# Kernel tuning notes

Hardware: AMD Instinct MI355X
Metric: run time of the kernel (lower is better)

The kernel has to match this reference:

```python
import jax, jax.numpy as jnp
import numpy as np


def _gcn_layer(x, W, b, src, dst, norm, n_nodes):
    # x: [N, Fin]; transform first (PyG GCNConv): h = x @ W
    h = x @ W  # [N, Fout]
    # gather-scale-scatter: out[d] += norm_e * h[s] over edges (incl. self loops)
    msgs = h[src] * norm[:, None]  # [E+N, Fout]
    agg = jax.ops.segment_sum(msgs, dst, num_segments=n_nodes)
    return agg + b


def setup_inputs() -> dict:
    key = jax.random.key(0)
    k1, k2, k3, k4 = jax.random.split(key, 4)
    N, E, F_IN, HID, OUT = 50000, 800000, 128, 256, 128
    x = jax.random.normal(k1, (N, F_IN), dtype=jnp.float32)
    edge_index = jax.random.randint(k2, (2, E), 0, N, dtype=jnp.int64)
    W1 = jax.random.normal(k3, (F_IN, HID), dtype=jnp.float32) / np.sqrt(F_IN)
    b1 = jnp.zeros((HID,), dtype=jnp.float32)
    W2 = jax.random.normal(k4, (HID, OUT), dtype=jnp.float32) / np.sqrt(HID)
    b2 = jnp.zeros((OUT,), dtype=jnp.float32)
    return {"x": x, "edge_index": edge_index, "W1": W1, "b1": b1, "W2": W2, "b2": b2}


def reference(x, edge_index, W1, b1, W2, b2):
    N = x.shape[0]
    # GCN normalization with self loops: A_hat = D^-1/2 (A + I) D^-1/2
    self_loops = jnp.arange(N, dtype=edge_index.dtype)
    src = jnp.concatenate([edge_index[0], self_loops])
    dst = jnp.concatenate([edge_index[1], self_loops])
    deg = jax.ops.segment_sum(jnp.ones_like(dst, dtype=x.dtype), dst, num_segments=N)
    dinv = jnp.where(deg > 0, jax.lax.rsqrt(deg), 0.0)
    norm = dinv[src] * dinv[dst]  # [E+N]
    h = _gcn_layer(x, W1, b1, src, dst, norm, N)
    h = jax.nn.relu(h)  # dropout is identity in eval mode
    out = _gcn_layer(h, W2, b2, src, dst, norm, N)
    return out  # unsupervised mode returns raw embeddings [N, 128]
```

## Files before the change

### kernel.cpp

```cpp
#include <hip/hip_runtime.h>
#include <hip/hip_bf16.h>


static constexpr int N_NODES = 50000;
static constexpr int N_EDGES = 800000;
static constexpr int F_IN = 128;
static constexpr int HID  = 256;
static constexpr int F_OUT = 128;
static constexpr int H2P  = 258;

typedef __attribute__((ext_vector_type(8))) short short8;
typedef __attribute__((ext_vector_type(4))) float f32x4;

__device__ __forceinline__ unsigned short f2bf(float f) {
    union { float f; unsigned u; } x; x.f = f;
    unsigned r = x.u + 0x7FFF + ((x.u >> 16) & 1);
    return (unsigned short)(r >> 16);
}
__device__ __forceinline__ float bf2f(unsigned short h) {
    union { unsigned u; float f; } x; x.u = ((unsigned)h) << 16;
    return x.f;
}

__global__ void deg_wt_kernel(const int* __restrict__ dst, int* __restrict__ deg,
                              int* __restrict__ pos, int E,
                              const float* __restrict__ W1, unsigned short* __restrict__ w1t,
                              const float* __restrict__ W2, unsigned short* __restrict__ w2t,
                              int EB, int NB1) {
    const int b = blockIdx.x;
    if (b < EB) {
        int i = b * 256 + threadIdx.x;
        if (i < E) pos[i] = atomicAdd(&deg[dst[i]], 1);
    } else if (b < EB + NB1) {
        int t = (b - EB) * 256 + threadIdx.x;
        if (t < F_IN * HID) {
            int n = t / F_IN, k = t - n * F_IN;
            w1t[t] = f2bf(W1[(size_t)k * HID + n]);
        }
    } else {
        int t = (b - EB - NB1) * 256 + threadIdx.x;
        if (t < HID * F_OUT) {
            int n = t / HID, k = t - n * HID;
            w2t[t] = f2bf(W2[(size_t)k * F_OUT + n]);
        }
    }
}

__global__ __launch_bounds__(256) void scan_reduce_dinv(const int* __restrict__ deg,
                                                        int* __restrict__ bsums,
                                                        float* __restrict__ dinv, int N) {
    int i = blockIdx.x * 256 + threadIdx.x;
    int v = (i < N) ? deg[i] : 0;
    if (i < N) dinv[i] = rsqrtf((float)(v + 1));
#pragma unroll
    for (int ofs = 32; ofs > 0; ofs >>= 1) v += __shfl_down(v, ofs);
    __shared__ int ws[4];
    if ((threadIdx.x & 63) == 0) ws[threadIdx.x >> 6] = v;
    __syncthreads();
    if (threadIdx.x == 0) bsums[blockIdx.x] = ws[0] + ws[1] + ws[2] + ws[3];
}

__global__ __launch_bounds__(256) void scan_final_scalex(const int* __restrict__ deg,
                                                         const int* __restrict__ bsums,
                                                         int* __restrict__ off, int N, int nb,
                                                         const float* __restrict__ x,
                                                         const float* __restrict__ dinv,
                                                         unsigned short* __restrict__ xs) {
    const int tid = threadIdx.x;
    if ((int)blockIdx.x >= nb) {
        int i = (blockIdx.x - nb) * 256 + tid;
        if (i < N_NODES * F_IN / 8) {
            float dv = dinv[i >> 4];
            float4 v0 = ((const float4*)x)[i * 2];
            float4 v1 = ((const float4*)x)[i * 2 + 1];
            short8 o;
            o[0] = (short)f2bf(v0.x * dv); o[1] = (short)f2bf(v0.y * dv);
            o[2] = (short)f2bf(v0.z * dv); o[3] = (short)f2bf(v0.w * dv);
            o[4] = (short)f2bf(v1.x * dv); o[5] = (short)f2bf(v1.y * dv);
            o[6] = (short)f2bf(v1.z * dv); o[7] = (short)f2bf(v1.w * dv);
            *(short8*)(xs + (size_t)i * 8) = o;
        }
        return;
    }
    __shared__ int bs[256];
    __shared__ int s[256];
    bs[tid] = (tid < nb) ? bsums[tid] : 0;
    const int i = blockIdx.x * 256 + tid;
    int v = (i < N) ? deg[i] : 0;
    s[tid] = v;
    __syncthreads();
    for (int ofs = 1; ofs < 256; ofs <<= 1) {
        int tb = (tid >= ofs) ? bs[tid - ofs] : 0;
        int tv = (tid >= ofs) ? s[tid - ofs] : 0;
        __syncthreads();
        bs[tid] += tb;
        s[tid] += tv;
        __syncthreads();
    }
    int bbase = (blockIdx.x == 0) ? 0 : bs[blockIdx.x - 1];
    int excl = (tid == 0) ? 0 : s[tid - 1];
    if (i <= N) off[i] = bbase + excl;
}

__global__ void scatter_kernel(const int* __restrict__ src, const int* __restrict__ dst,
                               const int* __restrict__ pos, const int* __restrict__ off,
                               int* __restrict__ csr, int E) {
    int i = blockIdx.x * blockDim.x + threadIdx.x;
    if (i < E) csr[off[dst[i]] + pos[i]] = src[i];
}

template <int MODE>
__global__ __launch_bounds__(256) void agg_bf16(const unsigned short* __restrict__ hs,
                                                const int* __restrict__ off,
                                                const int* __restrict__ csr,
                                                const float* __restrict__ dinv,
                                                const float* __restrict__ bias,
                                                void* __restrict__ outp, int N) {
    const int wid = threadIdx.x >> 6;
    const int n = blockIdx.x * 4 + wid;
    if (n >= N) return;
    const int lane = threadIdx.x & 63;
    const int lane16 = lane & 15;
    const int slot = lane >> 4;

    float va[8], vb[8], vc[8], vd[8];
#pragma unroll
    for (int j = 0; j < 8; j++) { va[j] = 0.f; vb[j] = 0.f; vc[j] = 0.f; vd[j] = 0.f; }

    if (slot == 0) {
        short8 s = *(const short8*)(hs + (size_t)n * 128 + lane16 * 8);
#pragma unroll
        for (int j = 0; j < 8; j++) va[j] = bf2f((unsigned short)s[j]);
    }

    const int e0 = off[n];
    const int e1 = off[n + 1];
    for (int e = e0 + slot; e < e1; e += 16) {
        const int i1 = e + 4, i2 = e + 8, i3 = e + 12;
        const float f1 = (i1 < e1) ? 1.f : 0.f;
        const float f2 = (i2 < e1) ? 1.f : 0.f;
        const float f3 = (i3 < e1) ? 1.f : 0.f;
        const int c1 = min(i1, e1 - 1), c2 = min(i2, e1 - 1), c3 = min(i3, e1 - 1);
        int s0 = csr[e];
        int s1 = csr[c1];
        int s2 = csr[c2];
        int s3 = csr[c3];
        short8 v0 = *(const short8*)(hs + (size_t)s0 * 128 + lane16 * 8);
        short8 v1 = *(const short8*)(hs + (size_t)s1 * 128 + lane16 * 8);
        short8 v2 = *(const short8*)(hs + (size_t)s2 * 128 + lane16 * 8);
        short8 v3 = *(const short8*)(hs + (size_t)s3 * 128 + lane16 * 8);
#pragma unroll
        for (int j = 0; j < 8; j++) va[j] += bf2f((unsigned short)v0[j]);
#pragma unroll
        for (int j = 0; j < 8; j++) vb[j] = fmaf(f1, bf2f((unsigned short)v1[j]), vb[j]);
#pragma unroll
        for (int j = 0; j < 8; j++) vc[j] = fmaf(f2, bf2f((unsigned short)v2[j]), vc[j]);
#pragma unroll
        for (int j = 0; j < 8; j++) vd[j] = fmaf(f3, bf2f((unsigned short)v3[j]), vd[j]);
    }
#pragma unroll
    for (int j = 0; j < 8; j++) va[j] += vb[j] + vc[j] + vd[j];

#pragma unroll
    for (int j = 0; j < 8; j++) va[j] += __shfl_down(va[j], 32);
#pragma unroll
    for (int j = 0; j < 8; j++) va[j] += __shfl_down(va[j], 16);

    if (lane < 16) {
        float dv = dinv[n];
        if (MODE == 0) {
            short8 o;
#pragma unroll
            for (int j = 0; j < 8; j++) o[j] = (short)f2bf(va[j] * dv);
            *(short8*)((unsigned short*)outp + (size_t)n * 128 + lane * 8) = o;
        } else {
            float* op = (float*)outp + (size_t)n * 128 + lane * 8;
            float4 o0, o1;
            o0.x = va[0] * dv + bias[lane * 8 + 0];
            o0.y = va[1] * dv + bias[lane * 8 + 1];
            o0.z = va[2] * dv + bias[lane * 8 + 2];
            o0.w = va[3] * dv + bias[lane * 8 + 3];
            o1.x = va[4] * dv + bias[lane * 8 + 4];
            o1.y = va[5] * dv + bias[lane * 8 + 5];
            o1.z = va[6] * dv + bias[lane * 8 + 6];
            o1.w = va[7] * dv + bias[lane * 8 + 7];
            ((float4*)op)[0] = o0;
            ((float4*)op)[1] = o1;
        }
    }
}

__global__ __launch_bounds__(512, 4) void gemm12(const unsigned short* __restrict__ Y,
                                                 const unsigned short* __restrict__ w1t,
                                                 const float* __restrict__ b1,
                                                 const unsigned short* __restrict__ w2t,
                                                 const float* __restrict__ dinv,
                                                 unsigned short* __restrict__ hs2, int M) {
    __shared__ unsigned short h2s[16 * H2P];

    const int wid = threadIdx.x >> 6;
    const int lane = threadIdx.x & 63;
    const int an = lane & 15;
    const int q = lane >> 4;

    short8 b1f[2][4];
    float bv[2];
#pragma unroll
    for (int t = 0; t < 2; t++) {
        const int col = wid * 32 + t * 16 + an;
        const unsigned short* wp = w1t + (size_t)col * F_IN + q * 8;
#pragma unroll
        for (int c = 0; c < 4; c++) b1f[t][c] = *(const short8*)(wp + c * 32);
        bv[t] = b1[col];
    }
    short8 b2f[8];
    const int colB = wid * 16 + an;
    {
        const unsigned short* wp = w2t + (size_t)colB * HID + q * 8;
#pragma unroll
        for (int c = 0; c < 8; c++) b2f[c] = *(const short8*)(wp + c * 32);
    }

    const int T = M >> 4;
    for (int t0 = blockIdx.x; t0 < T; t0 += gridDim.x) {
        const int m0 = t0 * 16;

        short8 a[4];
        {
            const unsigned short* yp = Y + (size_t)(m0 + an) * F_IN + q * 8;
#pragma unroll
            for (int c = 0; c < 4; c++) a[c] = *(const short8*)(yp + c * 32);
        }
        f32x4 accA0 = {0.f, 0.f, 0.f, 0.f};
        f32x4 accA1 = {0.f, 0.f, 0.f, 0.f};
#pragma unroll
        for (int c = 0; c < 4; c++) {
            accA0 = __builtin_amdgcn_mfma_f32_16x16x32_bf16(a[c], b1f[0][c], accA0, 0, 0, 0);
            accA1 = __builtin_amdgcn_mfma_f32_16x16x32_bf16(a[c], b1f[1][c], accA1, 0, 0, 0);
        }
        {
            const int c0 = wid * 32 + an;
            unsigned short* hrow = &h2s[(q * 4) * H2P];
#pragma unroll
            for (int rr = 0; rr < 4; rr++) {
                hrow[rr * H2P + c0]      = f2bf(fmaxf(accA0[rr] + bv[0], 0.f));
                hrow[rr * H2P + c0 + 16] = f2bf(fmaxf(accA1[rr] + bv[1], 0.f));
            }
        }
        __syncthreads();

        {
            short8 h[8];
            const unsigned short* hp = &h2s[an * H2P + q * 8];
#pragma unroll
            for (int c = 0; c < 8; c++) h[c] = *(const short8*)(hp + c * 32);
            f32x4 acc = {0.f, 0.f, 0.f, 0.f};
#pragma unroll
            for (int c = 0; c < 8; c++)
                acc = __builtin_amdgcn_mfma_f32_16x16x32_bf16(h[c], b2f[c], acc, 0, 0, 0);
            const float4 dv4 = ((const float4*)dinv)[(m0 >> 2) + q];
            unsigned short* op = hs2 + (size_t)(m0 + q * 4) * F_OUT + colB;
            op[0]         = f2bf(acc[0] * dv4.x);
            op[F_OUT]     = f2bf(acc[1] * dv4.y);
            op[2 * F_OUT] = f2bf(acc[2] * dv4.z);
            op[3 * F_OUT] = f2bf(acc[3] * dv4.w);
        }
        __syncthreads();
    }
}

extern "C" void kernel_launch(void* const* d_in, const int* in_sizes, int n_in,
                              void* d_out, int out_size, void* d_ws, size_t ws_size,
                              hipStream_t stream) {
    const float* x  = (const float*)d_in[0];
    const int*   ei = (const int*)d_in[1];
    const float* W1 = (const float*)d_in[2];
    const float* b1 = (const float*)d_in[3];
    const float* W2 = (const float*)d_in[4];
    const float* b2 = (const float*)d_in[5];

    const int N = N_NODES;
    const int E = N_EDGES;
    const int* srcp = ei;
    const int* dstp = ei + E;

    char* base = (char*)d_ws;
    size_t o = 0;
    auto alloc = [&](size_t bytes) {
        void* p = base + o;
        o = (o + bytes + 255) & ~(size_t)255;
        return p;
    };
    int*            deg  = (int*)alloc((size_t)N * 4);
    int*            offs = (int*)alloc((size_t)(N + 1) * 4);
    float*          dinv = (float*)alloc((size_t)N * 4);
    int*            bsum = (int*)alloc(256 * 4);
    int*            pos  = (int*)alloc((size_t)E * 4);
    int*            csr  = (int*)alloc((size_t)E * 4);
    unsigned short* xs   = (unsigned short*)alloc((size_t)N * F_IN * 2);
    unsigned short* Y    = (unsigned short*)alloc((size_t)N * F_IN * 2);
    unsigned short* w1t  = (unsigned short*)alloc((size_t)F_IN * HID * 2);
    unsigned short* w2t  = (unsigned short*)alloc((size_t)HID * F_OUT * 2);
    unsigned short* hs2  = xs;

    hipMemsetAsync(deg, 0, (size_t)N * 4, stream);

    const int NB  = (N + 256) / 256;
    const int NBX = (N * F_IN / 8 + 255) / 256;
    const int EB  = (E + 255) / 256;
    const int NB1 = (F_IN * HID + 255) / 256;
    const int NB2 = (HID * F_OUT + 255) / 256;

    deg_wt_kernel<<<EB + NB1 + NB2, 256, 0, stream>>>(dstp, deg, pos, E, W1, w1t, W2, w2t, EB, NB1);
    scan_reduce_dinv<<<NB, 256, 0, stream>>>(deg, bsum, dinv, N);
    scan_final_scalex<<<NB + NBX, 256, 0, stream>>>(deg, bsum, offs, N, NB, x, dinv, xs);
    scatter_kernel<<<EB, 256, 0, stream>>>(srcp, dstp, pos, offs, csr, E);

    agg_bf16<0><<<(N + 3) / 4, 256, 0, stream>>>(xs, offs, csr, dinv, nullptr, Y, N);
    gemm12<<<512, 512, 0, stream>>>(Y, w1t, b1, w2t, dinv, hs2, N);
    agg_bf16<1><<<(N + 3) / 4, 256, 0, stream>>>(hs2, offs, csr, dinv, b2, d_out, N);
}
```

Before: 250.7 us.

## Replicate bf16 weights and stage them through LDS in fused GEMM

```diff
diff --git a/kernel.cpp b/kernel.cpp
--- a/kernel.cpp
+++ b/kernel.cpp
@@ -8,6 +8,7 @@
 static constexpr int HID  = 256;
 static constexpr int F_OUT = 128;
 static constexpr int H2P  = 258;
+static constexpr int NREP = 16;
 
 typedef __attribute__((ext_vector_type(8))) short short8;
 typedef __attribute__((ext_vector_type(4))) float f32x4;
@@ -35,13 +36,17 @@
         int t = (b - EB) * 256 + threadIdx.x;
         if (t < F_IN * HID) {
             int n = t / F_IN, k = t - n * F_IN;
-            w1t[t] = f2bf(W1[(size_t)k * HID + n]);
+            unsigned short v = f2bf(W1[(size_t)k * HID + n]);
+#pragma unroll
+            for (int r = 0; r < NREP; r++) w1t[(size_t)r * F_IN * HID + t] = v;
         }
     } else {
         int t = (b - EB - NB1) * 256 + threadIdx.x;
         if (t < HID * F_OUT) {
             int n = t / HID, k = t - n * HID;
-            w2t[t] = f2bf(W2[(size_t)k * F_OUT + n]);
+            unsigned short v = f2bf(W2[(size_t)k * F_OUT + n]);
+#pragma unroll
+            for (int r = 0; r < NREP; r++) w2t[(size_t)r * HID * F_OUT + t] = v;
         }
     }
 }
@@ -196,30 +201,45 @@
                                                  const unsigned short* __restrict__ w2t,
                                                  const float* __restrict__ dinv,
                                                  unsigned short* __restrict__ hs2, int M) {
-    __shared__ unsigned short h2s[16 * H2P];
+    __shared__ unsigned short lds[F_IN * HID];
 
     const int wid = threadIdx.x >> 6;
     const int lane = threadIdx.x & 63;
     const int an = lane & 15;
     const int q = lane >> 4;
+    const int rep = blockIdx.x & (NREP - 1);
 
     short8 b1f[2][4];
     float bv[2];
-#pragma unroll
-    for (int t = 0; t < 2; t++) {
-        const int col = wid * 32 + t * 16 + an;
-        const unsigned short* wp = w1t + (size_t)col * F_IN + q * 8;
-#pragma unroll
-        for (int c = 0; c < 4; c++) b1f[t][c] = *(const short8*)(wp + c * 32);
-        bv[t] = b1[col];
+    {
+        const unsigned short* w1r = w1t + (size_t)rep * F_IN * HID;
+        for (int i = threadIdx.x; i < F_IN * HID / 8; i += 512)
+            *(short8*)(lds + i * 8) = *(const short8*)(w1r + (size_t)i * 8);
+        __syncthreads();
+#pragma unroll
+        for (int t = 0; t < 2; t++) {
+            const int col = wid * 32 + t * 16 + an;
+            const unsigned short* wp = lds + col * F_IN + q * 8;
+#pragma unroll
+            for (int c = 0; c < 4; c++) b1f[t][c] = *(const short8*)(wp + c * 32);
+            bv[t] = b1[col];
+        }
+        __syncthreads();
     }
     short8 b2f[8];
     const int colB = wid * 16 + an;
     {
-        const unsigned short* wp = w2t + (size_t)colB * HID + q * 8;
+        const unsigned short* w2r = w2t + (size_t)rep * HID * F_OUT;
+        for (int i = threadIdx.x; i < HID * F_OUT / 8; i += 512)
+            *(short8*)(lds + i * 8) = *(const short8*)(w2r + (size_t)i * 8);
+        __syncthreads();
+        const unsigned short* wp = lds + colB * HID + q * 8;
 #pragma unroll
         for (int c = 0; c < 8; c++) b2f[c] = *(const short8*)(wp + c * 32);
-    }
+        __syncthreads();
+    }
+
+    unsigned short* h2s = lds;
 
     const int T = M >> 4;
     for (int t0 = blockIdx.x; t0 < T; t0 += gridDim.x) {
@@ -299,8 +319,8 @@
     int*            csr  = (int*)alloc((size_t)E * 4);
     unsigned short* xs   = (unsigned short*)alloc((size_t)N * F_IN * 2);
     unsigned short* Y    = (unsigned short*)alloc((size_t)N * F_IN * 2);
-    unsigned short* w1t  = (unsigned short*)alloc((size_t)F_IN * HID * 2);
-    unsigned short* w2t  = (unsigned short*)alloc((size_t)HID * F_OUT * 2);
+    unsigned short* w1t  = (unsigned short*)alloc((size_t)NREP * F_IN * HID * 2);
+    unsigned short* w2t  = (unsigned short*)alloc((size_t)NREP * HID * F_OUT * 2);
     unsigned short* hs2  = xs;
 
     hipMemsetAsync(deg, 0, (size_t)N * 4, stream);
@@ -317,6 +337,6 @@
     scatter_kernel<<<EB, 256, 0, stream>>>(srcp, dstp, pos, offs, csr, E);
 
     agg_bf16<0><<<(N + 3) / 4, 256, 0, stream>>>(xs, offs, csr, dinv, nullptr, Y, N);
-    gemm12<<<512, 512, 0, stream>>>(Y, w1t, b1, w2t, dinv, hs2, N);
+    gemm12<<<256, 512, 0, stream>>>(Y, w1t, b1, w2t, dinv, hs2, N);
     agg_bf16<1><<<(N + 3) / 4, 256, 0, stream>>>(hs2, offs, csr, dinv, b2, d_out, N);
 }
```

New measurement: 257.7 us. 2.8% more time.
